# Kernel tuning notes

Measured on AMD Instinct MI355X. Metric: run time of the kernel, lower is better.

Reference implementation:

```python
import jax, jax.numpy as jnp
import numpy as np

N_NODES = 100000
N_EDGES = 1_600_000
D_IN = 64
DIM_H = 64


def _film_conv(x, src, dst, W_lin, W_film, b_film, W_skip, W_film_skip):
    """PyG FiLMConv, num_relations=1, aggr='mean', act=ReLU.
    lins/lin_skip have no bias; film has bias; film_skip has no bias."""
    n = x.shape[0]
    # skip/self term: (beta_s, gamma_s) = film_skip(x)
    beta_s, gamma_s = jnp.split(x @ W_film_skip, 2, axis=-1)
    out = jax.nn.relu(gamma_s * (x @ W_skip) + beta_s)
    # relation term: FiLM params from target node i, transform source node j
    beta, gamma = jnp.split(x @ W_film + b_film, 2, axis=-1)  # [N, H] each
    h = x @ W_lin                                             # [N, H]
    msg = jax.nn.relu(gamma[dst] * h[src] + beta[dst])        # [E, H] gather+FiLM
    agg = jax.ops.segment_sum(msg, dst, num_segments=n)       # scatter-sum
    deg = jax.ops.segment_sum(jnp.ones((src.shape[0],), msg.dtype), dst,
                              num_segments=n)
    return out + agg / jnp.maximum(deg, 1.0)[:, None]         # mean aggregation


def setup_inputs() -> dict:
    key = jax.random.key(0)
    ks = jax.random.split(key, 12)
    x = jax.random.normal(ks[0], (N_NODES, D_IN), dtype=jnp.float32)
    edge_index = jax.random.randint(ks[1], (2, N_EDGES), 0, N_NODES, dtype=jnp.int64)
    s_in = 1.0 / np.sqrt(D_IN)
    s_h = 1.0 / np.sqrt(DIM_H)
    params = {
        # layer 1 (D_IN -> DIM_H)
        "W_lin1": jax.random.normal(ks[2], (D_IN, DIM_H), jnp.float32) * s_in,
        "W_film1": jax.random.normal(ks[3], (D_IN, 2 * DIM_H), jnp.float32) * s_in,
        "b_film1": jnp.zeros((2 * DIM_H,), jnp.float32),
        "W_skip1": jax.random.normal(ks[4], (D_IN, DIM_H), jnp.float32) * s_in,
        "W_film_skip1": jax.random.normal(ks[5], (D_IN, 2 * DIM_H), jnp.float32) * s_in,
        # layer 2 (DIM_H -> DIM_H)
        "W_lin2": jax.random.normal(ks[6], (DIM_H, DIM_H), jnp.float32) * s_h,
        "W_film2": jax.random.normal(ks[7], (DIM_H, 2 * DIM_H), jnp.float32) * s_h,
        "b_film2": jnp.zeros((2 * DIM_H,), jnp.float32),
        "W_skip2": jax.random.normal(ks[8], (DIM_H, DIM_H), jnp.float32) * s_h,
        "W_film_skip2": jax.random.normal(ks[9], (DIM_H, 2 * DIM_H), jnp.float32) * s_h,
        # final head
        "W_out": jax.random.normal(ks[10], (DIM_H, 1), jnp.float32) * s_h,
        "b_out": jnp.zeros((1,), jnp.float32),
    }
    return {"x": x, "edge_index": edge_index, **params}


def reference(x, edge_index,
              W_lin1, W_film1, b_film1, W_skip1, W_film_skip1,
              W_lin2, W_film2, b_film2, W_skip2, W_film_skip2,
              W_out, b_out):
    src, dst = edge_index[0], edge_index[1]
    h = _film_conv(x, src, dst, W_lin1, W_film1, b_film1, W_skip1, W_film_skip1)
    h = jax.nn.leaky_relu(h, negative_slope=0.01)
    h = _film_conv(h, src, dst, W_lin2, W_film2, b_film2, W_skip2, W_film_skip2)
    h = jax.nn.leaky_relu(h, negative_slope=0.01)
    return h @ W_out + b_out  # [N, 1]
```

## Files before the change

kernel.cpp:

```cpp
#include <hip/hip_runtime.h>
#include <cstddef>


#define THREADS 256
#define NB 512
#define NPSHIFT 9
#define NPSZ 512
#define CAP 10240

typedef unsigned short u16;
typedef unsigned char u8;
typedef unsigned int u32;
typedef short bf16x8 __attribute__((ext_vector_type(8)));
typedef float f32x4 __attribute__((ext_vector_type(4)));
typedef float f32x2 __attribute__((ext_vector_type(2)));

__device__ __forceinline__ u16 f2b(float f) {
  u32 u = __float_as_uint(f);
  u32 r = (u + 0x7FFFu + ((u >> 16) & 1u)) >> 16;
  return (u16)r;
}
__device__ __forceinline__ float b2f(u16 u) {
  return __uint_as_float(((u32)u) << 16);
}
__device__ __forceinline__ u8 f2fp8(float v) {
  return (u8)(__builtin_amdgcn_cvt_pk_fp8_f32(v, v, 0, false) & 0xFF);
}

struct WSrc {
  const float* p;
  int ld;
  int off;
};
struct WPack {
  WSrc m[12];
};

__global__ __launch_bounds__(THREADS) void prep_and_scatter(
    WPack wp, u16* __restrict__ Wp, const int* __restrict__ src,
    const int* __restrict__ dst, int* __restrict__ gcur, u32* __restrict__ buck,
    int E, int CH, int P) {
  int b = blockIdx.x, t = threadIdx.x;
  if (b < 12) {
    WSrc ws = wp.m[b];
    u16* dstp = Wp + b * 4096;
#pragma unroll
    for (int i = 0; i < 16; ++i) {
      int e = t + 256 * i;
      int n = e >> 6, k = e & 63;
      float v = ws.p[(size_t)k * ws.ld + ws.off + n];
      dstp[e ^ ((n & 7) << 3)] = f2b(v);
    }
    return;
  }
  __shared__ int h[256];
  __shared__ int cur[256];
  int hb = b - 12;
  h[t] = 0;
  __syncthreads();
  int lo = hb * CH;
  int hi = min(lo + CH, E);
  if (lo >= E) return;
  for (int i = lo + t; i < hi; i += THREADS) atomicAdd(&h[dst[i] >> NPSHIFT], 1);
  __syncthreads();
  if (t < P) {
    int base = h[t] ? atomicAdd(&gcur[t], h[t]) : 0;
    cur[t] = t * CAP + base;
  }
  __syncthreads();
  for (int i = lo + t; i < hi; i += THREADS) {
    int d = dst[i];
    int pos = atomicAdd(&cur[d >> NPSHIFT], 1);
    buck[pos] = (u32)src[i] | ((u32)(d & (NPSZ - 1)) << 17);
  }
}

template <int INBF16>
__device__ __forceinline__ void gemm_body(
    u16* XT, u16* WT, int row0, const void* __restrict__ Xv, int N,
    const u16* __restrict__ WpL, const float* __restrict__ bfilm,
    u8* __restrict__ H8, u16* __restrict__ BETA, u16* __restrict__ GAMMA,
    u16* __restrict__ S) {
  int t = threadIdx.x;
  {
    int row = t >> 2, kq = (t & 3) * 16;
    int gr = row0 + row;
    uint4 w0 = {0, 0, 0, 0}, w1 = {0, 0, 0, 0};
    if (gr < N) {
      if (INBF16) {
        const uint4* xp = (const uint4*)((const u16*)Xv + (size_t)gr * 64 + kq);
        w0 = xp[0];
        w1 = xp[1];
      } else {
        const float* xp = (const float*)Xv + (size_t)gr * 64 + kq;
        float4 f0 = ((const float4*)xp)[0];
        float4 f1 = ((const float4*)xp)[1];
        float4 f2 = ((const float4*)xp)[2];
        float4 f3 = ((const float4*)xp)[3];
        w0.x = f2b(f0.x) | ((u32)f2b(f0.y) << 16);
        w0.y = f2b(f0.z) | ((u32)f2b(f0.w) << 16);
        w0.z = f2b(f1.x) | ((u32)f2b(f1.y) << 16);
        w0.w = f2b(f1.z) | ((u32)f2b(f1.w) << 16);
        w1.x = f2b(f2.x) | ((u32)f2b(f2.y) << 16);
        w1.y = f2b(f2.z) | ((u32)f2b(f2.w) << 16);
        w1.z = f2b(f3.x) | ((u32)f2b(f3.y) << 16);
        w1.w = f2b(f3.z) | ((u32)f2b(f3.w) << 16);
      }
    }
    int e = row * 64 + kq;
    int s = (row & 7) << 3;
    *(uint4*)&XT[e ^ s] = w0;
    *(uint4*)&XT[(e + 8) ^ s] = w1;
  }
  {
    const uint4* wsrc = (const uint4*)WpL;
    uint4* wdst = (uint4*)WT;
    for (int i = t; i < 1536; i += THREADS) wdst[i] = wsrc[i];
  }
  __syncthreads();

  int lane = t & 63, wid = t >> 6;
  int arow = wid * 16 + (lane & 15);
  int kb = (lane >> 4) << 3;
  int as = (arow & 7) << 3;
  bf16x8 A0 = *(const bf16x8*)&XT[(arow * 64 + kb) ^ as];
  bf16x8 A1 = *(const bf16x8*)&XT[(arow * 64 + 32 + kb) ^ as];

  auto bfrag = [&](int mat, int ct, int kk) -> bf16x8 {
    int n = ct * 16 + (lane & 15);
    int e = (n * 64 + kk * 32 + kb) ^ ((n & 7) << 3);
    return *(const bf16x8*)&WT[mat * 4096 + e];
  };

  const f32x4 z = {0.f, 0.f, 0.f, 0.f};
  int rbase = wid * 16 + ((lane >> 4) << 2);
  int cbase = lane & 15;

  f32x4 a0[4], a1[4], a2[4];
#pragma unroll
  for (int ct = 0; ct < 4; ++ct) {
    a0[ct] = z;
    a1[ct] = z;
    a2[ct] = z;
  }
#pragma unroll
  for (int ct = 0; ct < 4; ++ct) {
    a0[ct] = __builtin_amdgcn_mfma_f32_16x16x32_bf16(A0, bfrag(0, ct, 0), a0[ct], 0, 0, 0);
    a0[ct] = __builtin_amdgcn_mfma_f32_16x16x32_bf16(A1, bfrag(0, ct, 1), a0[ct], 0, 0, 0);
    a1[ct] = __builtin_amdgcn_mfma_f32_16x16x32_bf16(A0, bfrag(1, ct, 0), a1[ct], 0, 0, 0);
    a1[ct] = __builtin_amdgcn_mfma_f32_16x16x32_bf16(A1, bfrag(1, ct, 1), a1[ct], 0, 0, 0);
    a2[ct] = __builtin_amdgcn_mfma_f32_16x16x32_bf16(A0, bfrag(2, ct, 0), a2[ct], 0, 0, 0);
    a2[ct] = __builtin_amdgcn_mfma_f32_16x16x32_bf16(A1, bfrag(2, ct, 1), a2[ct], 0, 0, 0);
  }
  __syncthreads();
  {
    const uint4* wsrc = (const uint4*)WpL;
    uint4* wdst = (uint4*)WT;
    for (int i = t; i < 1536; i += THREADS) wdst[i] = wsrc[1536 + i];
  }
#pragma unroll
  for (int ct = 0; ct < 4; ++ct) {
    int c = ct * 16 + cbase;
#pragma unroll
    for (int r = 0; r < 4; ++r) {
      int gr = row0 + rbase + r;
      if (gr < N) {
        float v = fmaxf(fmaf(a2[ct][r], a0[ct][r], a1[ct][r]), 0.f);
        S[(size_t)gr * 64 + c] = f2b(v);
      }
    }
  }
  __syncthreads();

#pragma unroll
  for (int ct = 0; ct < 4; ++ct) {
    a0[ct] = z;
    a1[ct] = z;
    a2[ct] = z;
  }
#pragma unroll
  for (int ct = 0; ct < 4; ++ct) {
    a0[ct] = __builtin_amdgcn_mfma_f32_16x16x32_bf16(A0, bfrag(0, ct, 0), a0[ct], 0, 0, 0);
    a0[ct] = __builtin_amdgcn_mfma_f32_16x16x32_bf16(A1, bfrag(0, ct, 1), a0[ct], 0, 0, 0);
    a1[ct] = __builtin_amdgcn_mfma_f32_16x16x32_bf16(A0, bfrag(1, ct, 0), a1[ct], 0, 0, 0);
    a1[ct] = __builtin_amdgcn_mfma_f32_16x16x32_bf16(A1, bfrag(1, ct, 1), a1[ct], 0, 0, 0);
    a2[ct] = __builtin_amdgcn_mfma_f32_16x16x32_bf16(A0, bfrag(2, ct, 0), a2[ct], 0, 0, 0);
    a2[ct] = __builtin_amdgcn_mfma_f32_16x16x32_bf16(A1, bfrag(2, ct, 1), a2[ct], 0, 0, 0);
  }
#pragma unroll
  for (int ct = 0; ct < 4; ++ct) {
    int c = ct * 16 + cbase;
    float bb = bfilm[c];
    float bg = bfilm[64 + c];
#pragma unroll
    for (int r = 0; r < 4; ++r) {
      int gr = row0 + rbase + r;
      if (gr < N) {
        size_t o = (size_t)gr * 64 + c;
        H8[o] = f2fp8(a0[ct][r]);
        BETA[o] = f2b(a1[ct][r] + bb);
        GAMMA[o] = f2b(a2[ct][r] + bg);
      }
    }
  }
}

__device__ __forceinline__ void csr_body(
    char* smem, int p, const u32* __restrict__ buck, const int* __restrict__ gcur,
    int* __restrict__ begA, int* __restrict__ degA, int* __restrict__ csr,
    int* __restrict__ perm, int N, int P) {
  int* hA = (int*)smem;
  int* hB = hA + NPSZ;
  int* cur = hB + NPSZ;
  int* h64 = cur + NPSZ;
  int* c64 = h64 + 64;
  int t = threadIdx.x;
  int cnt = gcur[p];
  int pbase = p * CAP;
  hA[t] = 0;
  hA[t + 256] = 0;
  __syncthreads();
  for (int i = t; i < cnt; i += THREADS) atomicAdd(&hA[buck[pbase + i] >> 17], 1);
  __syncthreads();
  int deg0 = hA[t], deg1 = hA[t + 256];
  int* s = hA;
  int* d2 = hB;
  for (int off = 1; off < NPSZ; off <<= 1) {
#pragma unroll
    for (int r = 0; r < 2; ++r) {
      int idx = t + r * 256;
      int v = s[idx];
      if (idx >= off) v += s[idx - off];
      d2[idx] = v;
    }
    __syncthreads();
    int* tmp = s;
    s = d2;
    d2 = tmp;
  }
#pragma unroll
  for (int r = 0; r < 2; ++r) {
    int idx = t + r * 256;
    int excl = idx ? s[idx - 1] : 0;
    cur[idx] = excl;
    int node = (p << NPSHIFT) + idx;
    if (node < N) {
      begA[node] = pbase + excl;
      degA[node] = s[idx] - excl;
    }
  }
  __syncthreads();
  for (int i = t; i < cnt; i += THREADS) {
    u32 w = buck[pbase + i];
    int pos = atomicAdd(&cur[w >> 17], 1);
    csr[pbase + pos] = (int)(w & 0x1FFFFu);
  }
  {
    int padend = min(cnt + 160, CAP);
    for (int i = cnt + t; i < padend; i += THREADS) csr[pbase + i] = 0;
  }
  __syncthreads();
  if (t < 64) h64[t] = 0;
  __syncthreads();
  int b0 = min(deg0, 63), b1 = min(deg1, 63);
  atomicAdd(&h64[b0], 1);
  atomicAdd(&h64[b1], 1);
  __syncthreads();
  if (t == 0) {
    int run = 0;
    for (int i = 0; i < 64; ++i) {
      int v = h64[i];
      c64[i] = run;
      run += v;
    }
  }
  __syncthreads();
  int base_out = p << NPSHIFT;
  int pos0 = atomicAdd(&c64[b0], 1);
  perm[base_out + pos0] = base_out + t;
  int pos1 = atomicAdd(&c64[b1], 1);
  perm[base_out + pos1] = base_out + t + 256;
}

__global__ __launch_bounds__(THREADS) void build_and_gemm0(
    const u32* __restrict__ buck, const int* __restrict__ gcur,
    int* __restrict__ begA, int* __restrict__ degA, int* __restrict__ csr,
    int* __restrict__ perm, const float* __restrict__ X, int N,
    const u16* __restrict__ Wp, const float* __restrict__ bfilm,
    u8* __restrict__ H8, u16* __restrict__ BETA, u16* __restrict__ GAMMA,
    u16* __restrict__ S, int P) {
  __shared__ __align__(16) char smem[32768];
  if ((int)blockIdx.x < P) {
    csr_body(smem, blockIdx.x, buck, gcur, begA, degA, csr, perm, N, P);
  } else {
    u16* XT = (u16*)smem;
    u16* WT = XT + 4096;
    int row0 = ((int)blockIdx.x - P) * 64;
    gemm_body<0>(XT, WT, row0, X, N, Wp, bfilm, H8, BETA, GAMMA, S);
  }
}

__global__ __launch_bounds__(THREADS) void gemm_l2(
    const u16* __restrict__ X2, int N, const u16* __restrict__ WpL,
    const float* __restrict__ bfilm, u8* __restrict__ H8, u16* __restrict__ BETA,
    u16* __restrict__ GAMMA, u16* __restrict__ S) {
  __shared__ __align__(16) char smem[32768];
  u16* XT = (u16*)smem;
  u16* WT = XT + 4096;
  gemm_body<1>(XT, WT, blockIdx.x * 64, X2, N, WpL, bfilm, H8, BETA, GAMMA, S);
}

template <int FINAL>
__global__ __launch_bounds__(THREADS) void agg_kernel(
    const u8* __restrict__ H8, const u16* __restrict__ GAMMA,
    const u16* __restrict__ BETA, const u16* __restrict__ S,
    const int* __restrict__ begA, const int* __restrict__ degA,
    const int* __restrict__ csr, const int* __restrict__ perm,
    u16* __restrict__ Xn, const float* __restrict__ Wout,
    const float* __restrict__ bout, float* __restrict__ out, int N, int PCAP) {
  int wid = blockIdx.x * 4 + (threadIdx.x >> 6);
  int lane = threadIdx.x & 63;
  int q = lane >> 4;
  int fl = lane & 15;
  int node = perm[wid * 4 + q];
  bool valid = node < N;
  int nd = valid ? node : N - 1;
  int beg = begA[nd];
  int deg = valid ? degA[nd] : 0;
  int m = deg;
  m = max(m, __shfl_xor(m, 16, 64));
  m = max(m, __shfl_xor(m, 32, 64));

  size_t nb4 = (size_t)nd * 16 + fl;
  const uint2* G2 = (const uint2*)GAMMA;
  const uint2* B2 = (const uint2*)BETA;
  const u32* H1 = (const u32*)H8;
  const uint2* S2 = (const uint2*)S;
  uint2 gp = G2[nb4];
  uint2 bp = B2[nb4];

  auto unpA = [](u32 h) -> f32x2 {
    f32x2 r = {__uint_as_float(h << 16), __uint_as_float(h & 0xFFFF0000u)};
    return r;
  };
  f32x2 gA = unpA(gp.x), gB = unpA(gp.y);
  f32x2 bA = unpA(bp.x), bB = unpA(bp.y);
  const f32x2 zz = {0.f, 0.f};
  f32x2 accA = zz, accB = zz;
  int qb = q * 16;

  for (int c = 0; c < m; c += 16) {
    int li = beg + c + fl;
    int idxv = csr[min(li, PCAP - 1)];
    int nin = min(16, m - c);
#pragma unroll 4
    for (int u = 0; u < 16; u += 4) {
      if (u >= nin) break;
      int s0 = __shfl(idxv, qb + u + 0, 64);
      int s1 = __shfl(idxv, qb + u + 1, 64);
      int s2 = __shfl(idxv, qb + u + 2, 64);
      int s3 = __shfl(idxv, qb + u + 3, 64);
      u32 h0 = H1[(size_t)s0 * 16 + fl];
      u32 h1 = H1[(size_t)s1 * 16 + fl];
      u32 h2 = H1[(size_t)s2 * 16 + fl];
      u32 h3 = H1[(size_t)s3 * 16 + fl];
      int e0 = c + u;
      f32x2 lo, hi, mA, mB;
      bool ok;
      lo = __builtin_amdgcn_cvt_pk_f32_fp8((int)h0, false);
      hi = __builtin_amdgcn_cvt_pk_f32_fp8((int)h0, true);
      mA = __builtin_elementwise_max(__builtin_elementwise_fma(gA, lo, bA), zz);
      mB = __builtin_elementwise_max(__builtin_elementwise_fma(gB, hi, bB), zz);
      ok = e0 + 0 < deg;
      accA += ok ? mA : zz;
      accB += ok ? mB : zz;
      lo = __builtin_amdgcn_cvt_pk_f32_fp8((int)h1, false);
      hi = __builtin_amdgcn_cvt_pk_f32_fp8((int)h1, true);
      mA = __builtin_elementwise_max(__builtin_elementwise_fma(gA, lo, bA), zz);
      mB = __builtin_elementwise_max(__builtin_elementwise_fma(gB, hi, bB), zz);
      ok = e0 + 1 < deg;
      accA += ok ? mA : zz;
      accB += ok ? mB : zz;
      lo = __builtin_amdgcn_cvt_pk_f32_fp8((int)h2, false);
      hi = __builtin_amdgcn_cvt_pk_f32_fp8((int)h2, true);
      mA = __builtin_elementwise_max(__builtin_elementwise_fma(gA, lo, bA), zz);
      mB = __builtin_elementwise_max(__builtin_elementwise_fma(gB, hi, bB), zz);
      ok = e0 + 2 < deg;
      accA += ok ? mA : zz;
      accB += ok ? mB : zz;
      lo = __builtin_amdgcn_cvt_pk_f32_fp8((int)h3, false);
      hi = __builtin_amdgcn_cvt_pk_f32_fp8((int)h3, true);
      mA = __builtin_elementwise_max(__builtin_elementwise_fma(gA, lo, bA), zz);
      mB = __builtin_elementwise_max(__builtin_elementwise_fma(gB, hi, bB), zz);
      ok = e0 + 3 < deg;
      accA += ok ? mA : zz;
      accB += ok ? mB : zz;
    }
  }

  float inv = 1.f / fmaxf((float)deg, 1.f);
  uint2 sp = S2[nb4];
  f32x2 sA = unpA(sp.x), sB = unpA(sp.y);
  float v0 = fmaf(accA.x, inv, sA.x);
  float v1 = fmaf(accA.y, inv, sA.y);
  float v2 = fmaf(accB.x, inv, sB.x);
  float v3 = fmaf(accB.y, inv, sB.y);
  v0 = v0 > 0.f ? v0 : 0.01f * v0;
  v1 = v1 > 0.f ? v1 : 0.01f * v1;
  v2 = v2 > 0.f ? v2 : 0.01f * v2;
  v3 = v3 > 0.f ? v3 : 0.01f * v3;
  if (FINAL == 0) {
    if (valid) {
      uint2 pw;
      pw.x = (u32)f2b(v0) | ((u32)f2b(v1) << 16);
      pw.y = (u32)f2b(v2) | ((u32)f2b(v3) << 16);
      ((uint2*)Xn)[nb4] = pw;
    }
  } else {
    float4 w4 = ((const float4*)Wout)[fl];
    float v = fmaf(v0, w4.x, fmaf(v1, w4.y, fmaf(v2, w4.z, v3 * w4.w)));
#pragma unroll
    for (int off = 1; off < 16; off <<= 1) v += __shfl_xor(v, off, 64);
    if (valid && fl == 0) out[node] = v + bout[0];
  }
}

extern "C" void kernel_launch(void* const* d_in, const int* in_sizes, int n_in,
                              void* d_out, int out_size, void* d_ws, size_t ws_size,
                              hipStream_t stream) {
  const float* x = (const float*)d_in[0];
  const int* ei = (const int*)d_in[1];
  const float* Wlin1 = (const float*)d_in[2];
  const float* Wfilm1 = (const float*)d_in[3];
  const float* bfilm1 = (const float*)d_in[4];
  const float* Wskip1 = (const float*)d_in[5];
  const float* Wfs1 = (const float*)d_in[6];
  const float* Wlin2 = (const float*)d_in[7];
  const float* Wfilm2 = (const float*)d_in[8];
  const float* bfilm2 = (const float*)d_in[9];
  const float* Wskip2 = (const float*)d_in[10];
  const float* Wfs2 = (const float*)d_in[11];
  const float* Wout = (const float*)d_in[12];
  const float* bout = (const float*)d_in[13];

  int N = in_sizes[0] / 64;
  int E = in_sizes[1] / 2;
  const int* src = ei;
  const int* dst = ei + E;

  int P = (N + NPSZ - 1) >> NPSHIFT;
  int CH = (E + NB - 1) / NB;
  int NSLOT = P << NPSHIFT;
  int PCAP = P * CAP;

  size_t NF = (size_t)N * 64;
  char* p = (char*)d_ws;
  u8* H8 = (u8*)p;
  p += NF * 2;
  u16* BETA = (u16*)p;
  p += NF * 2;
  u16* GAMMA = (u16*)p;
  p += NF * 2;
  u16* S = (u16*)p;
  p += NF * 2;
  u16* X2 = (u16*)p;
  u32* buck = (u32*)p;
  size_t bsz = (size_t)PCAP * 4, xsz = NF * 2;
  p += (bsz > xsz ? bsz : xsz);
  u16* Wp = (u16*)p;
  p += 12 * 4096 * 2;
  int* begA = (int*)p;
  p += (size_t)NSLOT * 4;
  int* degA = (int*)p;
  p += (size_t)NSLOT * 4;
  int* csr = (int*)p;
  p += (size_t)PCAP * 4;
  int* perm = (int*)p;
  p += (size_t)NSLOT * 4;
  int* gcur = (int*)p;

  int gemm_blocks = (N + 63) / 64;
  int agg_blocks = NSLOT / 16;

  WPack wp;
  wp.m[0] = {Wskip1, 64, 0};
  wp.m[1] = {Wfs1, 128, 0};
  wp.m[2] = {Wfs1, 128, 64};
  wp.m[3] = {Wlin1, 64, 0};
  wp.m[4] = {Wfilm1, 128, 0};
  wp.m[5] = {Wfilm1, 128, 64};
  wp.m[6] = {Wskip2, 64, 0};
  wp.m[7] = {Wfs2, 128, 0};
  wp.m[8] = {Wfs2, 128, 64};
  wp.m[9] = {Wlin2, 64, 0};
  wp.m[10] = {Wfilm2, 128, 0};
  wp.m[11] = {Wfilm2, 128, 64};

  hipMemsetAsync(gcur, 0, 256 * sizeof(int), stream);
  prep_and_scatter<<<12 + NB, THREADS, 0, stream>>>(wp, Wp, src, dst, gcur, buck, E,
                                                    CH, P);
  build_and_gemm0<<<P + gemm_blocks, THREADS, 0, stream>>>(
      buck, gcur, begA, degA, csr, perm, x, N, Wp, bfilm1, H8, BETA, GAMMA, S, P);
  agg_kernel<0><<<agg_blocks, THREADS, 0, stream>>>(H8, GAMMA, BETA, S, begA, degA, csr,
                                                    perm, X2, nullptr, nullptr, nullptr,
                                                    N, PCAP);
  gemm_l2<<<gemm_blocks, THREADS, 0, stream>>>(X2, N, Wp + 6 * 4096, bfilm2, H8, BETA,
                                               GAMMA, S);
  agg_kernel<1><<<agg_blocks, THREADS, 0, stream>>>(H8, GAMMA, BETA, S, begA, degA, csr,
                                                    perm, nullptr, Wout, bout,
                                                    (float*)d_out, N, PCAP);
}
```

Measured before the change: 164.2 us.

## Stream weight matrices through double-buffered LDS to cut shared memory and raise occupancy

Instead of loading three 64x64 weight matrices at once into a 24KB LDS region, the GEMM body now streams one matrix at a time through a two-slot double buffer, loading the next matrix while computing the current one. Shared memory per block drops from 32KB to 24KB, and launch bounds now request 6 blocks per CU, which should raise occupancy and cut register pressure (accumulators are produced per matrix). In exchange there are more __syncthreads barriers (one per matrix), and the csr_body sharing the same smem must still fit in 24KB.

```diff
diff --git a/kernel.cpp b/kernel.cpp
--- a/kernel.cpp
+++ b/kernel.cpp
@@ -112,10 +112,10 @@
     *(uint4*)&XT[e ^ s] = w0;
     *(uint4*)&XT[(e + 8) ^ s] = w1;
   }
+  const uint4* wsrc = (const uint4*)WpL;
   {
-    const uint4* wsrc = (const uint4*)WpL;
     uint4* wdst = (uint4*)WT;
-    for (int i = t; i < 1536; i += THREADS) wdst[i] = wsrc[i];
+    for (int i = t; i < 512; i += THREADS) wdst[i] = wsrc[i];
   }
   __syncthreads();
 
@@ -126,82 +126,64 @@
   bf16x8 A0 = *(const bf16x8*)&XT[(arow * 64 + kb) ^ as];
   bf16x8 A1 = *(const bf16x8*)&XT[(arow * 64 + 32 + kb) ^ as];
 
-  auto bfrag = [&](int mat, int ct, int kk) -> bf16x8 {
-    int n = ct * 16 + (lane & 15);
-    int e = (n * 64 + kk * 32 + kb) ^ ((n & 7) << 3);
-    return *(const bf16x8*)&WT[mat * 4096 + e];
-  };
-
   const f32x4 z = {0.f, 0.f, 0.f, 0.f};
   int rbase = wid * 16 + ((lane >> 4) << 2);
   int cbase = lane & 15;
 
-  f32x4 a0[4], a1[4], a2[4];
-#pragma unroll
-  for (int ct = 0; ct < 4; ++ct) {
-    a0[ct] = z;
-    a1[ct] = z;
-    a2[ct] = z;
-  }
-#pragma unroll
-  for (int ct = 0; ct < 4; ++ct) {
-    a0[ct] = __builtin_amdgcn_mfma_f32_16x16x32_bf16(A0, bfrag(0, ct, 0), a0[ct], 0, 0, 0);
-    a0[ct] = __builtin_amdgcn_mfma_f32_16x16x32_bf16(A1, bfrag(0, ct, 1), a0[ct], 0, 0, 0);
-    a1[ct] = __builtin_amdgcn_mfma_f32_16x16x32_bf16(A0, bfrag(1, ct, 0), a1[ct], 0, 0, 0);
-    a1[ct] = __builtin_amdgcn_mfma_f32_16x16x32_bf16(A1, bfrag(1, ct, 1), a1[ct], 0, 0, 0);
-    a2[ct] = __builtin_amdgcn_mfma_f32_16x16x32_bf16(A0, bfrag(2, ct, 0), a2[ct], 0, 0, 0);
-    a2[ct] = __builtin_amdgcn_mfma_f32_16x16x32_bf16(A1, bfrag(2, ct, 1), a2[ct], 0, 0, 0);
-  }
-  __syncthreads();
-  {
-    const uint4* wsrc = (const uint4*)WpL;
-    uint4* wdst = (uint4*)WT;
-    for (int i = t; i < 1536; i += THREADS) wdst[i] = wsrc[1536 + i];
-  }
-#pragma unroll
-  for (int ct = 0; ct < 4; ++ct) {
-    int c = ct * 16 + cbase;
-#pragma unroll
-    for (int r = 0; r < 4; ++r) {
-      int gr = row0 + rbase + r;
-      if (gr < N) {
-        float v = fmaxf(fmaf(a2[ct][r], a0[ct][r], a1[ct][r]), 0.f);
-        S[(size_t)gr * 64 + c] = f2b(v);
+  f32x4 acc[3][4];
+
+#pragma unroll
+  for (int m = 0; m < 6; ++m) {
+    if (m < 5) {
+      uint4* wdst = (uint4*)(WT + ((m + 1) & 1) * 4096);
+      for (int i = t; i < 512; i += THREADS) wdst[i] = wsrc[(m + 1) * 512 + i];
+    }
+    int a = m % 3;
+    const u16* wb = WT + (m & 1) * 4096;
+#pragma unroll
+    for (int ct = 0; ct < 4; ++ct) {
+      int n = ct * 16 + cbase;
+      int sw = (n & 7) << 3;
+      bf16x8 B0 = *(const bf16x8*)&wb[(n * 64 + kb) ^ sw];
+      bf16x8 B1 = *(const bf16x8*)&wb[(n * 64 + 32 + kb) ^ sw];
+      f32x4 v = z;
+      v = __builtin_amdgcn_mfma_f32_16x16x32_bf16(A0, B0, v, 0, 0, 0);
+      v = __builtin_amdgcn_mfma_f32_16x16x32_bf16(A1, B1, v, 0, 0, 0);
+      acc[a][ct] = v;
+    }
+    if (m == 2) {
+#pragma unroll
+      for (int ct = 0; ct < 4; ++ct) {
+        int c = ct * 16 + cbase;
+#pragma unroll
+        for (int r = 0; r < 4; ++r) {
+          int gr = row0 + rbase + r;
+          if (gr < N) {
+            float v = fmaxf(fmaf(acc[2][ct][r], acc[0][ct][r], acc[1][ct][r]), 0.f);
+            S[(size_t)gr * 64 + c] = f2b(v);
+          }
+        }
       }
     }
-  }
-  __syncthreads();
-
-#pragma unroll
-  for (int ct = 0; ct < 4; ++ct) {
-    a0[ct] = z;
-    a1[ct] = z;
-    a2[ct] = z;
-  }
-#pragma unroll
-  for (int ct = 0; ct < 4; ++ct) {
-    a0[ct] = __builtin_amdgcn_mfma_f32_16x16x32_bf16(A0, bfrag(0, ct, 0), a0[ct], 0, 0, 0);
-    a0[ct] = __builtin_amdgcn_mfma_f32_16x16x32_bf16(A1, bfrag(0, ct, 1), a0[ct], 0, 0, 0);
-    a1[ct] = __builtin_amdgcn_mfma_f32_16x16x32_bf16(A0, bfrag(1, ct, 0), a1[ct], 0, 0, 0);
-    a1[ct] = __builtin_amdgcn_mfma_f32_16x16x32_bf16(A1, bfrag(1, ct, 1), a1[ct], 0, 0, 0);
-    a2[ct] = __builtin_amdgcn_mfma_f32_16x16x32_bf16(A0, bfrag(2, ct, 0), a2[ct], 0, 0, 0);
-    a2[ct] = __builtin_amdgcn_mfma_f32_16x16x32_bf16(A1, bfrag(2, ct, 1), a2[ct], 0, 0, 0);
-  }
-#pragma unroll
-  for (int ct = 0; ct < 4; ++ct) {
-    int c = ct * 16 + cbase;
-    float bb = bfilm[c];
-    float bg = bfilm[64 + c];
-#pragma unroll
-    for (int r = 0; r < 4; ++r) {
-      int gr = row0 + rbase + r;
-      if (gr < N) {
-        size_t o = (size_t)gr * 64 + c;
-        H8[o] = f2fp8(a0[ct][r]);
-        BETA[o] = f2b(a1[ct][r] + bb);
-        GAMMA[o] = f2b(a2[ct][r] + bg);
+    if (m == 5) {
+#pragma unroll
+      for (int ct = 0; ct < 4; ++ct) {
+        int c = ct * 16 + cbase;
+        float bb = bfilm[c];
+        float bg = bfilm[64 + c];
+#pragma unroll
+        for (int r = 0; r < 4; ++r) {
+          int gr = row0 + rbase + r;
+          if (gr < N) {
+            size_t o = (size_t)gr * 64 + c;
+            H8[o] = f2fp8(acc[0][ct][r]);
+            BETA[o] = f2b(acc[1][ct][r] + bb);
+            GAMMA[o] = f2b(acc[2][ct][r] + bg);
+          }
+        }
       }
     }
+    __syncthreads();
   }
 }
 
@@ -282,14 +264,14 @@
   perm[base_out + pos1] = base_out + t + 256;
 }
 
-__global__ __launch_bounds__(THREADS) void build_and_gemm0(
+__global__ __launch_bounds__(THREADS, 6) void build_and_gemm0(
     const u32* __restrict__ buck, const int* __restrict__ gcur,
     int* __restrict__ begA, int* __restrict__ degA, int* __restrict__ csr,
     int* __restrict__ perm, const float* __restrict__ X, int N,
     const u16* __restrict__ Wp, const float* __restrict__ bfilm,
     u8* __restrict__ H8, u16* __restrict__ BETA, u16* __restrict__ GAMMA,
     u16* __restrict__ S, int P) {
-  __shared__ __align__(16) char smem[32768];
+  __shared__ __align__(16) char smem[24576];
   if ((int)blockIdx.x < P) {
     csr_body(smem, blockIdx.x, buck, gcur, begA, degA, csr, perm, N, P);
   } else {
@@ -300,11 +282,11 @@
   }
 }
 
-__global__ __launch_bounds__(THREADS) void gemm_l2(
+__global__ __launch_bounds__(THREADS, 6) void gemm_l2(
     const u16* __restrict__ X2, int N, const u16* __restrict__ WpL,
     const float* __restrict__ bfilm, u8* __restrict__ H8, u16* __restrict__ BETA,
     u16* __restrict__ GAMMA, u16* __restrict__ S) {
-  __shared__ __align__(16) char smem[32768];
+  __shared__ __align__(16) char smem[24576];
   u16* XT = (u16*)smem;
   u16* WT = XT + 4096;
   gemm_body<1>(XT, WT, blockIdx.x * 64, X2, N, WpL, bfilm, H8, BETA, GAMMA, S);
```

Measured after the change: 171.4 us. 4.4% more time.
